# Kernel optimization log

Measured on AMD Instinct MI355X. Metric: run time of the kernel, lower is better.

The kernel has to match this reference:

```python
import jax, jax.numpy as jnp
import numpy as np

B, C, T, H, W, L = 4, 256, 8, 16, 16, 8
NO = 8                # num_offsets
D = C // NO           # per-head feature dim for offset/weight MLPs
EPS = 1e-5


def setup_inputs() -> dict:
    key = jax.random.key(0)
    ks = jax.random.split(key, 6)
    return {
        "features": jax.random.normal(ks[0], (B, C, T, H, W, L), jnp.float32),
        "pos": jax.random.normal(ks[1], (B, C, T, H, W, L), jnp.float32),
        "Wp": jax.random.normal(ks[2], (C, 3 * C), jnp.float32) * 0.02,  # 1x1x1 conv: 3C -> C
        "bp": jnp.zeros((C,), jnp.float32),
        "Wo": jax.random.normal(ks[3], (D, 3), jnp.float32) * 0.02,      # offset_embed Linear(d,3)
        "bo": jnp.zeros((3,), jnp.float32),
        "Ww": jax.random.normal(ks[4], (D, 2), jnp.float32) * 0.02,      # weight_embed Linear(d,2)
        "bw": jnp.zeros((2,), jnp.float32),
    }


def _trilinear_sample(feat, coords):
    """feat: (N,C,D1,D2,D3); coords: (N,G,3) in [-1,1] (axis order D1,D2,D3).
    align_corners=False, zeros padding (matches F.grid_sample semantics)."""
    N, Cc, D1, D2, D3 = feat.shape
    sizes = jnp.asarray([D1, D2, D3], feat.dtype)
    pix = ((coords + 1.0) * sizes - 1.0) * 0.5       # unnormalize to pixel coords
    lo = jnp.floor(pix)
    frac = pix - lo                                   # (N,G,3)
    lo = lo.astype(jnp.int32)
    dims = jnp.asarray([D1, D2, D3], jnp.int32)
    feat_flat = feat.reshape(N, Cc, D1 * D2 * D3)
    out = jnp.zeros((N, Cc, coords.shape[1]), feat.dtype)
    for dz in (0, 1):
        for dy in (0, 1):
            for dx in (0, 1):
                off = jnp.asarray([dz, dy, dx], jnp.int32)
                idx = lo + off                        # (N,G,3)
                wz = jnp.where(dz, frac[..., 0], 1.0 - frac[..., 0])
                wy = jnp.where(dy, frac[..., 1], 1.0 - frac[..., 1])
                wx = jnp.where(dx, frac[..., 2], 1.0 - frac[..., 2])
                wgt = wz * wy * wx                    # (N,G)
                valid = jnp.all((idx >= 0) & (idx < dims), axis=-1)
                idc = jnp.clip(idx, 0, dims - 1)
                lin = (idc[..., 0] * D2 + idc[..., 1]) * D3 + idc[..., 2]  # (N,G)
                vals = jnp.take_along_axis(feat_flat, lin[:, None, :], axis=2)  # (N,C,G)
                out = out + vals * (wgt * valid)[:, None, :]
    return out


def reference(features, pos, Wp, bp, Wo, bo, Ww, bw):
    Bv, Cv, Tv, Hv, Wv, Lv = features.shape
    BT = Bv * Tv
    feat = features.transpose(0, 2, 1, 3, 4, 5).reshape(BT, Cv, Hv, Wv, Lv)
    posr = pos.transpose(0, 2, 1, 3, 4, 5).reshape(BT, Cv, Hv, Wv, Lv)
    # global context + projection (1x1x1 conv over 3C channels) + ReLU
    glob = feat.mean(axis=(2, 3, 4), keepdims=True)
    src = jnp.concatenate([feat, posr, jnp.broadcast_to(glob, feat.shape)], axis=1)  # (BT,3C,H,W,L)
    proj = jax.nn.relu(jnp.einsum('nixyz,oi->noxyz', src, Wp) + bp[None, :, None, None, None])
    osrc = proj.transpose(0, 2, 3, 4, 1).reshape(BT, Hv, Wv, Lv, NO, D)
    # per-voxel per-head offsets in (0,1) and scalar weights
    offset = jax.nn.sigmoid(osrc @ Wo + bo)                      # (BT,H,W,L,NO,3)
    wgt = jax.nn.softmax(osrc @ Ww + bw, axis=-1)[..., 1]        # (BT,H,W,L,NO)
    # base flow field in [-1,1], deform in logit space, re-sigmoid
    base = jnp.stack(jnp.meshgrid(jnp.linspace(-1.0, 1.0, Hv),
                                  jnp.linspace(-1.0, 1.0, Wv),
                                  jnp.linspace(-1.0, 1.0, Lv), indexing='ij'), axis=-1)
    base01 = jnp.clip((base + 1.0) * 0.5, EPS, 1.0 - EPS)
    logit = jnp.log(base01 / (1.0 - base01))                     # (H,W,L,3)
    sp = jax.nn.sigmoid(logit[None, :, :, :, None, :] + offset)  # (BT,H,W,L,NO,3)
    grid = (sp * 2.0 - 1.0).transpose(0, 4, 1, 2, 3, 5).reshape(BT, NO * Hv * Wv * Lv, 3)
    sampled = _trilinear_sample(feat, grid).reshape(BT, Cv, NO, Hv, Wv, Lv)
    out = feat + jnp.einsum('bcnhwl,bhwln->bchwl', sampled, wgt)
    return out.reshape(Bv, Tv, Cv, Hv, Wv, Lv).transpose(0, 2, 1, 3, 4, 5)
```

## Files before the change

kernel.cpp:

```cpp
#include <hip/hip_runtime.h>

#define BB 4
#define CC 256
#define TT 8
#define HH 16
#define WW 16
#define LL 8
#define NO 8
#define DD 32
#define BT 32
#define VV 2048
#define KIN 512
#define EPS_ 1e-5f

typedef short bf16x8 __attribute__((ext_vector_type(8)));
typedef float f32x4 __attribute__((ext_vector_type(4)));
typedef float f32x2 __attribute__((ext_vector_type(2)));

static __device__ __forceinline__ float b2f(unsigned short u) {
    return __uint_as_float(((unsigned int)u) << 16);
}
static __device__ __forceinline__ float b2f_lo(unsigned int x) {
    return __uint_as_float(x << 16);
}
static __device__ __forceinline__ float b2f_hi(unsigned int x) {
    return __uint_as_float(x & 0xffff0000u);
}
static __device__ __forceinline__ unsigned short f2b(float f) {
    unsigned int x = __float_as_uint(f);
    unsigned int r = x + 0x7fffu + ((x >> 16) & 1u);
    return (unsigned short)(r >> 16);
}
static __device__ __forceinline__ unsigned int f2b_pk(float lo, float hi) {
    return (unsigned int)f2b(lo) | ((unsigned int)f2b(hi) << 16);
}
static __device__ __forceinline__ float sigm(float x) {
    return 1.0f / (1.0f + __expf(-x));
}
static __device__ __forceinline__ void glds16(const void* g, void* l) {
    __builtin_amdgcn_global_load_lds(
        (const __attribute__((address_space(1))) void*)g,
        (__attribute__((address_space(3))) void*)l, 16, 0, 0);
}
static __device__ __forceinline__ int xsw(int x, int j) {
    switch (j) {
        case 1:  return __builtin_amdgcn_update_dpp(0, x, 0xB1, 0xF, 0xF, true);
        case 2:  return __builtin_amdgcn_update_dpp(0, x, 0x4E, 0xF, 0xF, true);
        case 8:  return __builtin_amdgcn_update_dpp(0, x, 0x128, 0xF, 0xF, true);
        case 4:  return __builtin_amdgcn_ds_swizzle(x, 0x101F);
        case 16: return __builtin_amdgcn_ds_swizzle(x, 0x401F);
        default: return __shfl_xor(x, 32);
    }
}

__global__ __launch_bounds__(256) void k0_prep(const float* __restrict__ Wp,
                                               unsigned short* __restrict__ Wa) {
    int i = blockIdx.x * 256 + threadIdx.x;
    int o = i >> 9, k = i & 511;
    Wa[i] = f2b(Wp[o * 768 + k]);
}

__global__ __launch_bounds__(256) void k1_transpose(const float* __restrict__ features,
                                                    const float* __restrict__ pos,
                                                    unsigned short* __restrict__ srcT,
                                                    float* __restrict__ gpart) {
    const int vt  = blockIdx.x;
    const int ch  = blockIdx.y & 1;
    const int arr = blockIdx.y >> 1;
    const int n   = blockIdx.z;
    const int v0 = vt * 128;
    const int b = n >> 3, t = n & 7;
    const int tid = threadIdx.x;
    const int w = tid >> 6;
    const int lane = tid & 63;
    const int v16 = lane >> 2;
    const int cs  = lane & 3;

    __shared__ uint2 sg[128 * 33];

    const float* src = arr ? pos : features;
    const size_t cb = ((size_t)(b * CC + ch * 128 + w * 32) * TT + t) * (size_t)VV
                      + v0 + v16 * 4;

    float4 f[2][4][2];
    #pragma unroll
    for (int i = 0; i < 2; ++i)
        #pragma unroll
        for (int e = 0; e < 4; ++e)
            #pragma unroll
            for (int vh = 0; vh < 2; ++vh)
                f[i][e][vh] = *(const float4*)(src + cb
                                + (size_t)(i * 16 + cs * 4 + e) * (TT * VV) + vh * 64);

    #pragma unroll
    for (int i = 0; i < 2; ++i) {
        const int cq = w * 8 + i * 4 + cs;
        #pragma unroll
        for (int vh = 0; vh < 2; ++vh) {
            #pragma unroll
            for (int k = 0; k < 4; ++k) {
                const int v = vh * 64 + v16 * 4 + k;
                uint2 u;
                u.x = f2b_pk(((const float*)&f[i][0][vh])[k], ((const float*)&f[i][1][vh])[k]);
                u.y = f2b_pk(((const float*)&f[i][2][vh])[k], ((const float*)&f[i][3][vh])[k]);
                sg[v * 33 + cq] = u;
            }
        }
    }

    if (arr == 0) {
        float part[2][4];
        #pragma unroll
        for (int i = 0; i < 2; ++i)
            #pragma unroll
            for (int e = 0; e < 4; ++e) {
                part[i][e] = f[i][e][0].x + f[i][e][0].y + f[i][e][0].z + f[i][e][0].w
                           + f[i][e][1].x + f[i][e][1].y + f[i][e][1].z + f[i][e][1].w;
                #pragma unroll
                for (int m = 4; m < 64; m <<= 1)
                    part[i][e] += __shfl_xor(part[i][e], m);
            }
        if (lane < 4) {
            float* gp = gpart + ((size_t)n * 16 + vt) * CC + ch * 128 + w * 32 + cs * 4;
            *(float4*)gp        = make_float4(part[0][0], part[0][1], part[0][2], part[0][3]);
            *(float4*)(gp + 16) = make_float4(part[1][0], part[1][1], part[1][2], part[1][3]);
        }
    }
    __syncthreads();

    const int vh2 = tid >> 4;
    const int q   = tid & 15;
    unsigned short* ob = srcT + ((size_t)n * VV + v0) * KIN + arr * 256 + ch * 128 + q * 8;
    #pragma unroll
    for (int j = 0; j < 8; ++j) {
        const int v = j * 16 + vh2;
        uint2 lo = sg[v * 33 + q * 2];
        uint2 hi = sg[v * 33 + q * 2 + 1];
        uint4 o;
        o.x = lo.x; o.y = lo.y; o.z = hi.x; o.w = hi.y;
        *(uint4*)(ob + (size_t)v * KIN) = o;
    }
}

__global__ __launch_bounds__(256) void k2_gterm(const float* __restrict__ gpart,
                                                const float* __restrict__ Wp,
                                                const float* __restrict__ bp,
                                                float* __restrict__ gterm) {
    const int n = blockIdx.x;
    const int o = threadIdx.x;
    __shared__ float gl[CC];
    float s = 0.0f;
    const float* gp = gpart + (size_t)n * 16 * CC + o;
    #pragma unroll 8
    for (int vt = 0; vt < 16; ++vt) s += gp[vt * CC];
    gl[o] = s * (1.0f / (float)VV);
    __syncthreads();
    const float4* wrow = (const float4*)(Wp + (size_t)o * 768 + 512);
    const float4* g4 = (const float4*)gl;
    float acc = bp[o];
    #pragma unroll 8
    for (int c = 0; c < 64; ++c) {
        float4 w = wrow[c], g = g4[c];
        acc += w.x * g.x + w.y * g.y + w.z * g.z + w.w * g.w;
    }
    gterm[n * CC + o] = acc;
}

__global__ __launch_bounds__(256) void k3_gemm(const unsigned short* __restrict__ Wa,
                                               const unsigned short* __restrict__ srcT,
                                               const float* __restrict__ gterm,
                                               unsigned short* __restrict__ projT) {
    const int n  = blockIdx.x;
    const int mb = blockIdx.y;
    const int nb = blockIdx.z;
    const int tid = threadIdx.x;
    const int m0 = mb * 128, v0 = nb * 128;

    __shared__ short As[128 * 32];
    __shared__ short Bs[128 * 32];

    const int w = tid >> 6;
    const int lane = tid & 63;
    const int wm = w >> 1, wn = w & 1;
    const int lr = lane & 15, lq = lane >> 4;

    f32x4 acc[4][4];
    #pragma unroll
    for (int i = 0; i < 4; ++i)
        #pragma unroll
        for (int j = 0; j < 4; ++j)
            acc[i][j] = (f32x4){0.f, 0.f, 0.f, 0.f};

    const int rsub = lane >> 2;
    const int ksub = (lane & 3) * 8;
    const unsigned short* agp = Wa   + (size_t)(m0 + w * 16 + rsub) * KIN + ksub;
    const unsigned short* bgp = srcT + ((size_t)n * VV + v0 + w * 16 + rsub) * KIN + ksub;
    short* alds0 = &As[(w * 16) * 32];
    short* alds1 = &As[(64 + w * 16) * 32];
    short* blds0 = &Bs[(w * 16) * 32];
    short* blds1 = &Bs[(64 + w * 16) * 32];

    for (int k0 = 0; k0 < KIN; k0 += 32) {
        __syncthreads();
        glds16(agp + k0,                    alds0);
        glds16(agp + k0 + (size_t)64 * KIN, alds1);
        glds16(bgp + k0,                    blds0);
        glds16(bgp + k0 + (size_t)64 * KIN, blds1);
        __syncthreads();

        bf16x8 af[4], bf[4];
        #pragma unroll
        for (int i = 0; i < 4; ++i)
            af[i] = *(const bf16x8*)&As[(wm * 64 + i * 16 + lr) * 32 + lq * 8];
        #pragma unroll
        for (int j = 0; j < 4; ++j)
            bf[j] = *(const bf16x8*)&Bs[(wn * 64 + j * 16 + lr) * 32 + lq * 8];
        #pragma unroll
        for (int i = 0; i < 4; ++i)
            #pragma unroll
            for (int j = 0; j < 4; ++j)
                acc[i][j] = __builtin_amdgcn_mfma_f32_16x16x32_bf16(af[i], bf[j], acc[i][j], 0, 0, 0);
    }

    #pragma unroll
    for (int i = 0; i < 4; ++i) {
        const int og = m0 + wm * 64 + i * 16 + lq * 4;
        float4 g = *(const float4*)(gterm + n * CC + og);
        #pragma unroll
        for (int j = 0; j < 4; ++j) {
            const int vg = v0 + wn * 64 + j * 16 + lr;
            float x0 = fmaxf(acc[i][j][0] + g.x, 0.0f);
            float x1 = fmaxf(acc[i][j][1] + g.y, 0.0f);
            float x2 = fmaxf(acc[i][j][2] + g.z, 0.0f);
            float x3 = fmaxf(acc[i][j][3] + g.w, 0.0f);
            ushort4 st;
            st.x = f2b(x0); st.y = f2b(x1); st.z = f2b(x2); st.w = f2b(x3);
            *(ushort4*)&projT[((size_t)n * VV + vg) * CC + og] = st;
        }
    }
}

__global__ __launch_bounds__(256) void k4_coef(const unsigned short* __restrict__ projT,
                                               const float* __restrict__ Wo,
                                               const float* __restrict__ bo,
                                               const float* __restrict__ Ww,
                                               const float* __restrict__ bw,
                                               int2* __restrict__ pairs) {
    __shared__ float sWo[96], sWw[64], sb[5];
    const int tid = threadIdx.x;
    if (tid < 96) sWo[tid] = Wo[tid];
    if (tid < 64) sWw[tid] = Ww[tid];
    if (tid < 3)  sb[tid] = bo[tid];
    if (tid < 2)  sb[3 + tid] = bw[tid];
    __syncthreads();

    const int g = blockIdx.x * 256 + tid;
    const int n = g >> 14;
    const int rem = g & 16383;
    const int v = rem >> 3;
    const int hd = rem & 7;

    const uint4* up = (const uint4*)(projT + ((size_t)n * VV + v) * CC + hd * DD);
    float osrc[32];
    #pragma unroll
    for (int q = 0; q < 4; ++q) {
        uint4 u = up[q];
        unsigned int ws4[4] = {u.x, u.y, u.z, u.w};
        #pragma unroll
        for (int e = 0; e < 4; ++e) {
            osrc[q * 8 + e * 2]     = b2f_lo(ws4[e]);
            osrc[q * 8 + e * 2 + 1] = b2f_hi(ws4[e]);
        }
    }

    float o0 = sb[0], o1 = sb[1], o2 = sb[2];
    float zw = sb[4] - sb[3];
    #pragma unroll
    for (int d = 0; d < DD; ++d) {
        float t = osrc[d];
        o0 += t * sWo[3 * d + 0];
        o1 += t * sWo[3 * d + 1];
        o2 += t * sWo[3 * d + 2];
        zw += t * (sWw[2 * d + 1] - sWw[2 * d]);
    }
    const float wgt = sigm(zw);

    const int h = v >> 7, w = (v >> 3) & 15, l = v & 7;
    float ph = fminf(fmaxf(h * (1.0f / 15.0f), EPS_), 1.0f - EPS_);
    float pw = fminf(fmaxf(w * (1.0f / 15.0f), EPS_), 1.0f - EPS_);
    float pl = fminf(fmaxf(l * (1.0f / 7.0f),  EPS_), 1.0f - EPS_);
    float lh = __logf(ph / (1.0f - ph));
    float lw = __logf(pw / (1.0f - pw));
    float ll = __logf(pl / (1.0f - pl));

    float sph = sigm(lh + sigm(o0));
    float spw = sigm(lw + sigm(o1));
    float spl = sigm(ll + sigm(o2));
    float pixh = sph * 16.0f - 0.5f;
    float pixw = spw * 16.0f - 0.5f;
    float pixl = spl * 8.0f  - 0.5f;

    float flh = floorf(pixh), flw = floorf(pixw), fll = floorf(pixl);
    float fh = pixh - flh, fw = pixw - flw, fl = pixl - fll;
    int ih = (int)flh, iw = (int)flw, il = (int)fll;

    int2* pp = pairs + (size_t)g * 8;
    #pragma unroll
    for (int dz = 0; dz < 2; ++dz)
        #pragma unroll
        for (int dy = 0; dy < 2; ++dy)
            #pragma unroll
            for (int dx = 0; dx < 2; ++dx) {
                int iz = ih + dz, iy = iw + dy, ix = il + dx;
                float wt = (dz ? fh : 1.0f - fh) * (dy ? fw : 1.0f - fw) * (dx ? fl : 1.0f - fl) * wgt;
                bool valid = ((unsigned)iz < 16u) && ((unsigned)iy < 16u) && ((unsigned)ix < 8u);
                int lin = valid ? (((iz * 16 + iy) * 8 + ix) << 10) : 0;
                float wv2 = valid ? wt : 0.0f;
                pp[dz * 4 + dy * 2 + dx] = make_int2(lin, __float_as_int(wv2));
            }
}

__global__ __launch_bounds__(256) void k5_gather(const unsigned short* __restrict__ srcT,
                                                 const int2* __restrict__ pairs,
                                                 unsigned short* __restrict__ res) {
    __shared__ int   sK[4 * 64];
    __shared__ float sW[4 * 64];
    const int tid = threadIdx.x;
    const int wid = tid >> 6;
    const int lane = tid & 63;
    const int gv = blockIdx.x * 4 + wid;
    const int n = gv >> 11;
    const int v = gv & 2047;

    int2 q = pairs[(size_t)gv * 64 + lane];
    int key = q.x;
    float w = __int_as_float(q.y);

    #pragma unroll
    for (int k = 2; k <= 64; k <<= 1) {
        #pragma unroll
        for (int j = k >> 1; j > 0; j >>= 1) {
            int pk = xsw(key, j);
            float pw = __int_as_float(xsw(__float_as_int(w), j));
            bool keepMin = (((lane & k) == 0) == ((lane & j) == 0));
            bool take = keepMin ? (pk < key) : (pk > key);
            if (take) { key = pk; w = pw; }
        }
    }
    #pragma unroll
    for (int d = 1; d < 64; d <<= 1) {
        float tw = __shfl_up(w, d);
        int   tk = __shfl_up(key, d);
        if (lane >= d && tk == key) w += tw;
    }
    int nk = __shfl_down(key, 1);
    bool tail = (lane == 63) || (nk != key);
    unsigned long long mask = __ballot(tail);
    int cnt = __popcll(mask);
    int cidx = __popcll(mask & ((1ull << lane) - 1ull));

    sK[wid * 64 + lane] = 0;
    sW[wid * 64 + lane] = 0.0f;
    __syncthreads();
    if (tail) { sK[wid * 64 + cidx] = key; sW[wid * 64 + cidx] = w; }
    __syncthreads();
    int ck = sK[wid * 64 + lane];
    float cw = sW[wid * 64 + lane];

    const char* slabB = (const char*)srcT + (size_t)n * VV * KIN * 2 + lane * 8;
    f32x2 a01 = (f32x2){0.f, 0.f}, a23 = (f32x2){0.f, 0.f};
    const int iters = (cnt + 7) & ~7;
    #pragma unroll 1
    for (int e = 0; e < iters; e += 8) {
        uint2 f[8]; float wv[8];
        #pragma unroll
        for (int u = 0; u < 8; ++u) {
            int rk = __builtin_amdgcn_readlane(ck, e + u);
            wv[u] = __uint_as_float(
                        __builtin_amdgcn_readlane(__float_as_uint(cw), e + u));
            f[u] = *(const uint2*)(slabB + (unsigned)rk);
        }
        #pragma unroll
        for (int u = 0; u < 8; ++u) {
            a01 += wv[u] * (f32x2){b2f_lo(f[u].x), b2f_hi(f[u].x)};
            a23 += wv[u] * (f32x2){b2f_lo(f[u].y), b2f_hi(f[u].y)};
        }
    }

    uint2 st;
    st.x = f2b_pk(a01.x, a01.y);
    st.y = f2b_pk(a23.x, a23.y);
    *(uint2*)&res[((size_t)n * VV + v) * CC + lane * 4] = st;
}

__global__ __launch_bounds__(256) void k6_final(const float* __restrict__ features,
                                                const unsigned short* __restrict__ res,
                                                float* __restrict__ out) {
    const int n = blockIdx.x;
    const int c0 = blockIdx.y * 128;
    const int v0 = blockIdx.z * 64;
    const int b = n >> 3, t = n & 7;
    const int tid = threadIdx.x;

    __shared__ uint2 t6[64 * 33];

    const int lr = tid >> 5;
    const int cp = tid & 31;
    #pragma unroll
    for (int p = 0; p < 8; ++p) {
        const int r = p * 8 + lr;
        t6[r * 33 + cp] = *(const uint2*)&res[((size_t)n * VV + v0 + r) * CC + c0 + cp * 4];
    }
    __syncthreads();

    const unsigned short* t6s = (const unsigned short*)t6;
    const int tx = tid & 63;
    const int cl0 = tid >> 6;
    #pragma unroll 8
    for (int p = 0; p < 32; ++p) {
        const int cl = p * 4 + cl0;
        const int c = c0 + cl;
        size_t oidx = (((size_t)b * CC + c) * TT + t) * VV + v0 + tx;
        unsigned short val = t6s[(tx * 33 + (cl >> 2)) * 4 + (cl & 3)];
        out[oidx] = features[oidx] + b2f(val);
    }
}

extern "C" void kernel_launch(void* const* d_in, const int* in_sizes, int n_in,
                              void* d_out, int out_size, void* d_ws, size_t ws_size,
                              hipStream_t stream) {
    (void)in_sizes; (void)n_in; (void)out_size; (void)ws_size;
    const float* features = (const float*)d_in[0];
    const float* pos      = (const float*)d_in[1];
    const float* Wp       = (const float*)d_in[2];
    const float* bp       = (const float*)d_in[3];
    const float* Wo       = (const float*)d_in[4];
    const float* bo       = (const float*)d_in[5];
    const float* Ww       = (const float*)d_in[6];
    const float* bw       = (const float*)d_in[7];
    float* out = (float*)d_out;

    char* ws = (char*)d_ws;
    unsigned short* srcT  = (unsigned short*)ws;
    unsigned short* Wa    = (unsigned short*)(ws + 67108864);
    float*          gterm = (float*)(ws + 67403776);
    unsigned short* projT = (unsigned short*)(ws + 67436544);
    int2*           pairs = (int2*)(ws + 100990976);
    float*          gpart = (float*)(ws + 100990976);
    unsigned short* res   = projT;

    k0_prep<<<512, 256, 0, stream>>>(Wp, Wa);
    k1_transpose<<<dim3(16, 4, 32), 256, 0, stream>>>(features, pos, srcT, gpart);
    k2_gterm<<<32, 256, 0, stream>>>(gpart, Wp, bp, gterm);
    k3_gemm<<<dim3(32, 2, 16), 256, 0, stream>>>(Wa, srcT, gterm, projT);
    k4_coef<<<2048, 256, 0, stream>>>(projT, Wo, bo, Ww, bw, pairs);
    k5_gather<<<16384, 256, 0, stream>>>(srcT, pairs, res);
    k6_final<<<dim3(32, 2, 32), 256, 0, stream>>>(features, res, out);
}
```

Measured before the change: 318.0 us.

## Fuse offset/weight coefficient computation into the trilinear gather kernel

Removes the separate k4_coef kernel and computes offsets, weights and corner keys inside the gather kernel. Each lane reads 4 channels of its voxel's projected features and reduces the per-head dot products with xor-shuffles across 8-lane groups. Each lane then emits one of the 8 trilinear corners directly as its sort key. This drops the global write and re-read of the intermediate pairs buffer and one kernel launch. In exchange the gather kernel carries extra ALU work and shuffles, and reads projT in place before overwriting the same row as res.

```diff
diff --git a/kernel.cpp b/kernel.cpp
--- a/kernel.cpp
+++ b/kernel.cpp
@@ -240,111 +240,77 @@
     }
 }
 
-__global__ __launch_bounds__(256) void k4_coef(const unsigned short* __restrict__ projT,
-                                               const float* __restrict__ Wo,
-                                               const float* __restrict__ bo,
-                                               const float* __restrict__ Ww,
-                                               const float* __restrict__ bw,
-                                               int2* __restrict__ pairs) {
-    __shared__ float sWo[96], sWw[64], sb[5];
-    const int tid = threadIdx.x;
-    if (tid < 96) sWo[tid] = Wo[tid];
-    if (tid < 64) sWw[tid] = Ww[tid];
-    if (tid < 3)  sb[tid] = bo[tid];
-    if (tid < 2)  sb[3 + tid] = bw[tid];
-    __syncthreads();
-
-    const int g = blockIdx.x * 256 + tid;
-    const int n = g >> 14;
-    const int rem = g & 16383;
-    const int v = rem >> 3;
-    const int hd = rem & 7;
-
-    const uint4* up = (const uint4*)(projT + ((size_t)n * VV + v) * CC + hd * DD);
-    float osrc[32];
-    #pragma unroll
-    for (int q = 0; q < 4; ++q) {
-        uint4 u = up[q];
-        unsigned int ws4[4] = {u.x, u.y, u.z, u.w};
-        #pragma unroll
-        for (int e = 0; e < 4; ++e) {
-            osrc[q * 8 + e * 2]     = b2f_lo(ws4[e]);
-            osrc[q * 8 + e * 2 + 1] = b2f_hi(ws4[e]);
-        }
-    }
-
-    float o0 = sb[0], o1 = sb[1], o2 = sb[2];
-    float zw = sb[4] - sb[3];
-    #pragma unroll
-    for (int d = 0; d < DD; ++d) {
-        float t = osrc[d];
-        o0 += t * sWo[3 * d + 0];
-        o1 += t * sWo[3 * d + 1];
-        o2 += t * sWo[3 * d + 2];
-        zw += t * (sWw[2 * d + 1] - sWw[2 * d]);
-    }
-    const float wgt = sigm(zw);
-
-    const int h = v >> 7, w = (v >> 3) & 15, l = v & 7;
-    float ph = fminf(fmaxf(h * (1.0f / 15.0f), EPS_), 1.0f - EPS_);
-    float pw = fminf(fmaxf(w * (1.0f / 15.0f), EPS_), 1.0f - EPS_);
-    float pl = fminf(fmaxf(l * (1.0f / 7.0f),  EPS_), 1.0f - EPS_);
-    float lh = __logf(ph / (1.0f - ph));
-    float lw = __logf(pw / (1.0f - pw));
-    float ll = __logf(pl / (1.0f - pl));
-
-    float sph = sigm(lh + sigm(o0));
-    float spw = sigm(lw + sigm(o1));
-    float spl = sigm(ll + sigm(o2));
-    float pixh = sph * 16.0f - 0.5f;
-    float pixw = spw * 16.0f - 0.5f;
-    float pixl = spl * 8.0f  - 0.5f;
-
-    float flh = floorf(pixh), flw = floorf(pixw), fll = floorf(pixl);
-    float fh = pixh - flh, fw = pixw - flw, fl = pixl - fll;
-    int ih = (int)flh, iw = (int)flw, il = (int)fll;
-
-    int2* pp = pairs + (size_t)g * 8;
-    #pragma unroll
-    for (int dz = 0; dz < 2; ++dz)
-        #pragma unroll
-        for (int dy = 0; dy < 2; ++dy)
-            #pragma unroll
-            for (int dx = 0; dx < 2; ++dx) {
-                int iz = ih + dz, iy = iw + dy, ix = il + dx;
-                float wt = (dz ? fh : 1.0f - fh) * (dy ? fw : 1.0f - fw) * (dx ? fl : 1.0f - fl) * wgt;
-                bool valid = ((unsigned)iz < 16u) && ((unsigned)iy < 16u) && ((unsigned)ix < 8u);
-                int lin = valid ? (((iz * 16 + iy) * 8 + ix) << 10) : 0;
-                float wv2 = valid ? wt : 0.0f;
-                pp[dz * 4 + dy * 2 + dx] = make_int2(lin, __float_as_int(wv2));
-            }
-}
-
-__global__ __launch_bounds__(256) void k5_gather(const unsigned short* __restrict__ srcT,
-                                                 const int2* __restrict__ pairs,
-                                                 unsigned short* __restrict__ res) {
+__global__ __launch_bounds__(256) void k5_fused(const unsigned short* __restrict__ projT,
+                                                const unsigned short* __restrict__ srcT,
+                                                const float* __restrict__ Wo,
+                                                const float* __restrict__ bo,
+                                                const float* __restrict__ Ww,
+                                                const float* __restrict__ bw,
+                                                unsigned short* __restrict__ res) {
+    __shared__ float sWo[96], sWd[32], sb[5];
     __shared__ int   sK[4 * 64];
     __shared__ float sW[4 * 64];
     const int tid = threadIdx.x;
     const int wid = tid >> 6;
     const int lane = tid & 63;
+    if (tid < 96) sWo[tid] = Wo[tid];
+    if (tid < 32) sWd[tid] = Ww[2 * tid + 1] - Ww[2 * tid];
+    if (tid < 3)  sb[tid] = bo[tid];
+    if (tid < 2)  sb[3 + tid] = bw[tid];
+    __syncthreads();
+
     const int gv = blockIdx.x * 4 + wid;
     const int n = gv >> 11;
     const int v = gv & 2047;
 
-    int2 q = pairs[(size_t)gv * 64 + lane];
-    int key = q.x;
-    float w = __int_as_float(q.y);
+    const int hd = lane >> 3;
+    const int s  = lane & 7;
+
+    uint2 pr = *(const uint2*)(projT + ((size_t)n * VV + v) * CC + lane * 4);
+    float t0 = b2f_lo(pr.x), t1 = b2f_hi(pr.x), t2 = b2f_lo(pr.y), t3 = b2f_hi(pr.y);
+    const int d0 = s * 4;
+    float o0 = t0 * sWo[3 * d0 + 0] + t1 * sWo[3 * d0 + 3] + t2 * sWo[3 * d0 + 6] + t3 * sWo[3 * d0 + 9];
+    float o1 = t0 * sWo[3 * d0 + 1] + t1 * sWo[3 * d0 + 4] + t2 * sWo[3 * d0 + 7] + t3 * sWo[3 * d0 + 10];
+    float o2 = t0 * sWo[3 * d0 + 2] + t1 * sWo[3 * d0 + 5] + t2 * sWo[3 * d0 + 8] + t3 * sWo[3 * d0 + 11];
+    float zw = t0 * sWd[d0] + t1 * sWd[d0 + 1] + t2 * sWd[d0 + 2] + t3 * sWd[d0 + 3];
+    #pragma unroll
+    for (int m = 1; m < 8; m <<= 1) {
+        o0 += __shfl_xor(o0, m);
+        o1 += __shfl_xor(o1, m);
+        o2 += __shfl_xor(o2, m);
+        zw += __shfl_xor(zw, m);
+    }
+    o0 += sb[0]; o1 += sb[1]; o2 += sb[2];
+    const float wgt = sigm(zw + sb[4] - sb[3]);
+
+    const int h = v >> 7, wv_ = (v >> 3) & 15, l = v & 7;
+    float ph = fminf(fmaxf(h   * (1.0f / 15.0f), EPS_), 1.0f - EPS_);
+    float pw = fminf(fmaxf(wv_ * (1.0f / 15.0f), EPS_), 1.0f - EPS_);
+    float pl = fminf(fmaxf(l   * (1.0f / 7.0f),  EPS_), 1.0f - EPS_);
+    float sph = sigm(__logf(ph / (1.0f - ph)) + sigm(o0));
+    float spw = sigm(__logf(pw / (1.0f - pw)) + sigm(o1));
+    float spl = sigm(__logf(pl / (1.0f - pl)) + sigm(o2));
+    float pixh = sph * 16.0f - 0.5f;
+    float pixw = spw * 16.0f - 0.5f;
+    float pixl = spl * 8.0f  - 0.5f;
+    float flh = floorf(pixh), flw = floorf(pixw), fll = floorf(pixl);
+    float fh = pixh - flh, fw = pixw - flw, fl = pixl - fll;
+    const int dz = s >> 2, dy = (s >> 1) & 1, dx = s & 1;
+    int iz = (int)flh + dz, iy = (int)flw + dy, ix = (int)fll + dx;
+    float wt = (dz ? fh : 1.0f - fh) * (dy ? fw : 1.0f - fw) * (dx ? fl : 1.0f - fl) * wgt;
+    bool valid = ((unsigned)iz < 16u) && ((unsigned)iy < 16u) && ((unsigned)ix < 8u);
+    int key = valid ? (((iz * 16 + iy) * 8 + ix) << 10) : 0;
+    float w = valid ? wt : 0.0f;
 
     #pragma unroll
     for (int k = 2; k <= 64; k <<= 1) {
         #pragma unroll
         for (int j = k >> 1; j > 0; j >>= 1) {
             int pk = xsw(key, j);
-            float pw = __int_as_float(xsw(__float_as_int(w), j));
+            float pw2 = __int_as_float(xsw(__float_as_int(w), j));
             bool keepMin = (((lane & k) == 0) == ((lane & j) == 0));
             bool take = keepMin ? (pk < key) : (pk > key);
-            if (take) { key = pk; w = pw; }
+            if (take) { key = pk; w = pw2; }
         }
     }
     #pragma unroll
@@ -372,18 +338,18 @@
     const int iters = (cnt + 7) & ~7;
     #pragma unroll 1
     for (int e = 0; e < iters; e += 8) {
-        uint2 f[8]; float wv[8];
+        uint2 f[8]; float wvv[8];
         #pragma unroll
         for (int u = 0; u < 8; ++u) {
             int rk = __builtin_amdgcn_readlane(ck, e + u);
-            wv[u] = __uint_as_float(
+            wvv[u] = __uint_as_float(
                         __builtin_amdgcn_readlane(__float_as_uint(cw), e + u));
             f[u] = *(const uint2*)(slabB + (unsigned)rk);
         }
         #pragma unroll
         for (int u = 0; u < 8; ++u) {
-            a01 += wv[u] * (f32x2){b2f_lo(f[u].x), b2f_hi(f[u].x)};
-            a23 += wv[u] * (f32x2){b2f_lo(f[u].y), b2f_hi(f[u].y)};
+            a01 += wvv[u] * (f32x2){b2f_lo(f[u].x), b2f_hi(f[u].x)};
+            a23 += wvv[u] * (f32x2){b2f_lo(f[u].y), b2f_hi(f[u].y)};
         }
     }
 
@@ -445,7 +411,6 @@
     unsigned short* Wa    = (unsigned short*)(ws + 67108864);
     float*          gterm = (float*)(ws + 67403776);
     unsigned short* projT = (unsigned short*)(ws + 67436544);
-    int2*           pairs = (int2*)(ws + 100990976);
     float*          gpart = (float*)(ws + 100990976);
     unsigned short* res   = projT;
 
@@ -453,7 +418,6 @@
     k1_transpose<<<dim3(16, 4, 32), 256, 0, stream>>>(features, pos, srcT, gpart);
     k2_gterm<<<32, 256, 0, stream>>>(gpart, Wp, bp, gterm);
     k3_gemm<<<dim3(32, 2, 16), 256, 0, stream>>>(Wa, srcT, gterm, projT);
-    k4_coef<<<2048, 256, 0, stream>>>(projT, Wo, bo, Ww, bw, pairs);
-    k5_gather<<<16384, 256, 0, stream>>>(srcT, pairs, res);
+    k5_fused<<<16384, 256, 0, stream>>>(projT, srcT, Wo, bo, Ww, bw, res);
     k6_final<<<dim3(32, 2, 32), 256, 0, stream>>>(features, res, out);
 }
```

Measured after the change: 318.5 us. Within noise of the previous version (+0.2%).
